# Kernel tuning notes

Measured on AMD Instinct MI355X. Metric: run time of the kernel, lower is better.

## Reference

```python
import jax, jax.numpy as jnp
import numpy as np

N, E, R = 50000, 500000, 3
IN, HID, OUT = 128, 128, 128
NEG_SLOPE = 0.2


def setup_inputs() -> dict:
    key = jax.random.key(0)
    ks = jax.random.split(key, 16)
    g = lambda i, shape: jax.random.normal(ks[i], shape, jnp.float32) * 0.1
    return {
        "x": jax.random.normal(ks[0], (N, IN), jnp.float32),
        "edge_index": jax.random.randint(ks[1], (2, E), 0, N, jnp.int32),
        "edge_type": jax.random.randint(ks[2], (E,), 0, R, jnp.int32),
        "edge_attr": jax.random.normal(ks[3], (E, 1), jnp.float32),
        # conv1 params (RGATConv: per-relation weight, q/k/e attention vectors, edge lin, bias)
        "w1": g(4, (R, IN, HID)), "q1": g(5, (HID, 1)), "k1": g(6, (HID, 1)),
        "le1": g(7, (1, HID)), "e1": g(8, (HID, 1)), "b1": jnp.zeros((HID,), jnp.float32),
        # conv2 params
        "w2": g(9, (R, HID, OUT)), "q2": g(10, (OUT, 1)), "k2": g(11, (OUT, 1)),
        "le2": g(12, (1, OUT)), "e2": g(13, (OUT, 1)), "b2": jnp.zeros((OUT,), jnp.float32),
    }


def _rgat_conv(x, src, dst, edge_type, edge_attr, w, q, k, le, e, b):
    """PyG RGATConv: heads=1, dim=1, additive-self-attention, across-relation softmax."""
    n = x.shape[0]
    # Per-relation linear at node level (equiv. to per-edge bmm with w[edge_type])
    xw = jnp.einsum('ni,rio->rno', x, w)            # [R, N, C]
    x_j = xw[edge_type, src]                          # [E, C] transformed source feats
    x_i = xw[edge_type, dst]                          # [E, C] transformed target feats
    # additive attention logits: q(x_i) + k(x_j) + e(lin_edge(edge_attr))
    alpha = x_i @ q + x_j @ k + (edge_attr @ le) @ e  # [E, 1]
    alpha = jax.nn.leaky_relu(alpha, negative_slope=NEG_SLOPE)
    # across-relation softmax over incoming edges of each target node
    amax = jax.ops.segment_max(alpha, dst, num_segments=n)
    amax = jnp.where(jnp.isfinite(amax), amax, 0.0)   # empty segments -> 0
    ex = jnp.exp(alpha - amax[dst])
    denom = jax.ops.segment_sum(ex, dst, num_segments=n)
    alpha = ex / (denom[dst] + 1e-16)
    # weighted scatter-add aggregation, then bias (concat=True, heads=1)
    out = jax.ops.segment_sum(alpha * x_j, dst, num_segments=n)  # [N, C]
    return out + b


def reference(x, edge_index, edge_type, edge_attr,
              w1, q1, k1, le1, e1, b1,
              w2, q2, k2, le2, e2, b2):
    src, dst = edge_index[0], edge_index[1]
    h = jax.nn.relu(_rgat_conv(x, src, dst, edge_type, edge_attr, w1, q1, k1, le1, e1, b1))
    return _rgat_conv(h, src, dst, edge_type, edge_attr, w2, q2, k2, le2, e2, b2)
```

## Files before the change

kernel.cpp:

```cpp
#include <hip/hip_runtime.h>
#include <hip/hip_bf16.h>
#include <math.h>

typedef __bf16 bf16x8 __attribute__((ext_vector_type(8)));
typedef float f32x4 __attribute__((ext_vector_type(4)));

#define CDIM 128

__global__ void sentinel_kernel(float* outf) {
  if (threadIdx.x == 0) outf[0] = 12345.0f;
}

__global__ __launch_bounds__(256) void prep_hist_kernel(
    const float* __restrict__ w1, const float* __restrict__ w2,
    __hip_bfloat16* __restrict__ wt,
    const float* __restrict__ le1, const float* __restrict__ e1,
    const float* __restrict__ le2, const float* __restrict__ e2,
    float* __restrict__ outc, const int* __restrict__ dstv,
    int* __restrict__ deg, int perW, int E) {
  const int b = blockIdx.x;
  const int tid = threadIdx.x;
  if (b < 48) {
    int t = b * 256 + tid;
    if (t >= perW * 2) return;
    const float* w = (t < perW) ? w1 : w2;
    int tt = (t < perW) ? t : t - perW;
    int r = tt >> 11;
    int rem = tt & 2047;
    int kb = rem >> 7;
    int o = rem & 127;
    const float* wr = w + ((size_t)r << 14);
    union { __hip_bfloat16 h[8]; int4 v; } u;
#pragma unroll
    for (int j = 0; j < 8; ++j)
      u.h[j] = __float2bfloat16(wr[(size_t)(kb * 8 + j) * CDIM + o]);
    *reinterpret_cast<int4*>(wt + (size_t)t * 8) = u.v;
  } else if (b == 48) {
    if (tid < 64) {
      float v1 = le1[tid] * e1[tid] + le1[tid + 64] * e1[tid + 64];
      float v2 = le2[tid] * e2[tid] + le2[tid + 64] * e2[tid + 64];
#pragma unroll
      for (int off = 32; off > 0; off >>= 1) {
        v1 += __shfl_xor(v1, off, 64);
        v2 += __shfl_xor(v2, off, 64);
      }
      if (tid == 0) { outc[0] = v1; outc[1] = v2; }
    }
  } else {
    int e0 = (b - 49) * 1024 + tid * 4;
    if (e0 + 3 < E) {
      int4 d4 = *reinterpret_cast<const int4*>(&dstv[e0]);
      atomicAdd(&deg[d4.x], 1);
      atomicAdd(&deg[d4.y], 1);
      atomicAdd(&deg[d4.z], 1);
      atomicAdd(&deg[d4.w], 1);
    } else {
      for (int t = 0; t < 4; ++t) {
        int e = e0 + t;
        if (e < E) atomicAdd(&deg[dstv[e]], 1);
      }
    }
  }
}


__global__ __launch_bounds__(256) void scan1_kernel(const int* __restrict__ deg,
                                                    int* __restrict__ rowptr,
                                                    int* __restrict__ partials, int n) {
  __shared__ int sh[256];
  int t = threadIdx.x;
  int base = blockIdx.x * 1024;
  int idx = base + t * 4;
  int v[4]; int s = 0;
#pragma unroll
  for (int j = 0; j < 4; ++j) { v[j] = (idx + j < n) ? deg[idx + j] : 0; s += v[j]; }
  sh[t] = s;
  __syncthreads();
  for (int off = 1; off < 256; off <<= 1) {
    int x = (t >= off) ? sh[t - off] : 0;
    __syncthreads();
    sh[t] += x;
    __syncthreads();
  }
  int excl = sh[t] - s;
  if (t == 255) partials[blockIdx.x] = sh[255];
  int run = excl;
#pragma unroll
  for (int j = 0; j < 4; ++j) {
    if (idx + j < n) rowptr[idx + j] = run;
    run += v[j];
  }
}

__global__ __launch_bounds__(256) void scan3_kernel(int* __restrict__ rowptr,
                                                    int* __restrict__ cursor,
                                                    const int* __restrict__ partials,
                                                    int nb, int n, int E) {
  __shared__ int spfx[64];
  int t = threadIdx.x;
  if (t < 64) {
    int pv = (t < nb) ? partials[t] : 0;
    int v = pv;
#pragma unroll
    for (int off = 1; off < 64; off <<= 1) {
      int u = __shfl_up(v, off, 64);
      if (t >= off) v += u;
    }
    spfx[t] = v - pv;
  }
  __syncthreads();
  int i = blockIdx.x * 256 + t;
  if (i < n) {
    int v = rowptr[i] + spfx[i >> 10];
    rowptr[i] = v;
    cursor[i] = v;
  } else if (i == n) {
    rowptr[n] = E;
  }
}

__device__ __forceinline__ void gemm_body64(
    int tb, const float* __restrict__ xin, const __hip_bfloat16* __restrict__ wt,
    const float* __restrict__ qv, const float* __restrict__ kv,
    __hip_bfloat16* __restrict__ xwout, float* __restrict__ sq,
    float* __restrict__ sk, int n, __hip_bfloat16* wlds, float* qls, float* kls) {
  const int tid = threadIdx.x;
  const int wave = tid >> 6, lane = tid & 63;
  const int quad = lane >> 4, c16 = lane & 15;
  const int m = tb * 64 + wave * 16 + c16;
  const bool ok = m < n;

  if (tid < 128) qls[tid] = qv[tid];
  else kls[tid - 128] = kv[tid - 128];

  bf16x8 zf;
#pragma unroll
  for (int j = 0; j < 8; ++j) zf[j] = (__bf16)0.0f;

  bf16x8 af[4];
#pragma unroll
  for (int ks = 0; ks < 4; ++ks) {
    if (ok) {
      const float* xp = xin + (size_t)m * CDIM + ks * 32 + quad * 8;
      f32x4 x0 = *reinterpret_cast<const f32x4*>(xp);
      f32x4 x1 = *reinterpret_cast<const f32x4*>(xp + 4);
      bf16x8 a;
#pragma unroll
      for (int j = 0; j < 4; ++j) { a[j] = (__bf16)x0[j]; a[4 + j] = (__bf16)x1[j]; }
      af[ks] = a;
    } else {
      af[ks] = zf;
    }
  }

  for (int r = 0; r < 3; ++r) {
    if (r) __syncthreads();
    {
      const int4* src = reinterpret_cast<const int4*>(wt + ((size_t)r << 14));
      int4* dst = reinterpret_cast<int4*>(wlds);
#pragma unroll
      for (int i = 0; i < 8; ++i) dst[tid + i * 256] = src[tid + i * 256];
    }
    __syncthreads();

    f32x4 acc[8];
#pragma unroll
    for (int ot = 0; ot < 8; ++ot) acc[ot] = (f32x4){0.f, 0.f, 0.f, 0.f};

#pragma unroll
    for (int ks = 0; ks < 4; ++ks) {
#pragma unroll
      for (int ot = 0; ot < 8; ++ot) {
        bf16x8 b = *reinterpret_cast<const bf16x8*>(
            &wlds[(((ks * 4 + quad) * 128) + ot * 16 + c16) * 8]);
        acc[ot] = __builtin_amdgcn_mfma_f32_16x16x32_bf16(b, af[ks], acc[ot], 0, 0, 0);
      }
    }

    __hip_bfloat16* rp = xwout + (((size_t)r * n + m) << 7) + quad * 4;
    float s_q = 0.f, s_k = 0.f;
#pragma unroll
    for (int ot = 0; ot < 8; ++ot) {
      f32x4 a = acc[ot];
      f32x4 q4 = *reinterpret_cast<const f32x4*>(&qls[ot * 16 + quad * 4]);
      f32x4 k4 = *reinterpret_cast<const f32x4*>(&kls[ot * 16 + quad * 4]);
      s_q += a[0] * q4[0] + a[1] * q4[1] + a[2] * q4[2] + a[3] * q4[3];
      s_k += a[0] * k4[0] + a[1] * k4[1] + a[2] * k4[2] + a[3] * k4[3];
      if (ok) {
        union { __hip_bfloat16 b4[4]; uint2 u; } pk;
#pragma unroll
        for (int t = 0; t < 4; ++t) pk.b4[t] = __float2bfloat16(a[t]);
        *reinterpret_cast<uint2*>(rp + ot * 16) = pk.u;
      }
    }
    s_q += __shfl_xor(s_q, 16, 64);
    s_q += __shfl_xor(s_q, 32, 64);
    s_k += __shfl_xor(s_k, 16, 64);
    s_k += __shfl_xor(s_k, 32, 64);
    if (quad == 0 && ok) {
      sq[(size_t)r * n + m] = s_q;
      sk[(size_t)r * n + m] = s_k;
    }
  }
}

__global__ __launch_bounds__(256) void gemm_scatter_kernel(
    const float* __restrict__ xin, const __hip_bfloat16* __restrict__ wt,
    const float* __restrict__ qv, const float* __restrict__ kv,
    __hip_bfloat16* __restrict__ xwout, float* __restrict__ sq, float* __restrict__ sk,
    const int* __restrict__ srcv, const int* __restrict__ dstv,
    const int* __restrict__ etype, const float* __restrict__ eattr,
    int* __restrict__ cursor, int2* __restrict__ kattr,
    int NT, int n, int E) {
  __shared__ __hip_bfloat16 wlds[16 * 128 * 8];
  __shared__ float qls[128], kls[128];
  const int b = blockIdx.x;
  if (b < NT) {
    gemm_body64(b, xin, wt, qv, kv, xwout, sq, sk, n, wlds, qls, kls);
  } else {
    int e0 = (b - NT) * 1024 + threadIdx.x * 4;
    if (e0 + 3 < E) {
      int4 s4 = *reinterpret_cast<const int4*>(&srcv[e0]);
      int4 d4 = *reinterpret_cast<const int4*>(&dstv[e0]);
      int4 t4 = *reinterpret_cast<const int4*>(&etype[e0]);
      float4 a4 = *reinterpret_cast<const float4*>(&eattr[e0]);
      int p0 = atomicAdd(&cursor[d4.x], 1);
      kattr[p0] = make_int2(t4.x * n + s4.x, __float_as_int(a4.x));
      int p1 = atomicAdd(&cursor[d4.y], 1);
      kattr[p1] = make_int2(t4.y * n + s4.y, __float_as_int(a4.y));
      int p2 = atomicAdd(&cursor[d4.z], 1);
      kattr[p2] = make_int2(t4.z * n + s4.z, __float_as_int(a4.z));
      int p3 = atomicAdd(&cursor[d4.w], 1);
      kattr[p3] = make_int2(t4.w * n + s4.w, __float_as_int(a4.w));
    } else {
      for (int t = 0; t < 4; ++t) {
        int e = e0 + t;
        if (e < E) {
          int p = atomicAdd(&cursor[dstv[e]], 1);
          kattr[p] = make_int2(etype[e] * n + srcv[e], __float_as_int(eattr[e]));
        }
      }
    }
  }
}

__global__ __launch_bounds__(256) void gemm_xw_kernel(
    const float* __restrict__ xin, const __hip_bfloat16* __restrict__ wt,
    const float* __restrict__ qv, const float* __restrict__ kv,
    __hip_bfloat16* __restrict__ xwout, float* __restrict__ sq, float* __restrict__ sk,
    int n) {
  __shared__ __hip_bfloat16 wlds[16 * 128 * 8];
  __shared__ float qls[128], kls[128];
  gemm_body64(blockIdx.x, xin, wt, qv, kv, xwout, sq, sk, n, wlds, qls, kls);
}

__global__ __launch_bounds__(256) void aggregate_kernel(
    const int* __restrict__ rowptr, const int2* __restrict__ kattr,
    const float* __restrict__ sq, const float* __restrict__ sk,
    const __hip_bfloat16* __restrict__ xw, const float* __restrict__ bias,
    const float* __restrict__ cscal, float* __restrict__ out, int n, int do_relu) {
  const int wave = threadIdx.x >> 6, lane = threadIdx.x & 63;
  const int g = lane >> 4;
  const int sub = lane & 15;
  const int node = blockIdx.x * 16 + wave * 4 + g;
  if (node >= n) return;
  const float c = cscal[0];
  const int n2 = n * 2;

  const int start = rowptr[node];
  const int deg = rowptr[node + 1] - start;
  const float s0 = sq[node], s1 = sq[n + node], s2 = sq[n2 + node];

  float acc[8];
#pragma unroll
  for (int t = 0; t < 8; ++t) acc[t] = 0.f;
  float den = 0.f;

  for (int j0 = 0; j0 < deg; j0 += 4) {
    int2 ka[4];
#pragma unroll
    for (int t = 0; t < 4; ++t) {
      int idx = j0 + t;
      ka[t] = kattr[start + (idx < deg ? idx : 0)];
    }
    float w[4];
    bf16x8 f[4];
#pragma unroll
    for (int t = 0; t < 4; ++t) {
      int kk = ka[t].x;
      float sv = (kk >= n2) ? s2 : ((kk >= n) ? s1 : s0);
      float l = sv + sk[kk] + c * __int_as_float(ka[t].y);
      l = l > 0.f ? l : 0.2f * l;
      w[t] = (j0 + t < deg) ? __expf(l) : 0.f;
      f[t] = *reinterpret_cast<const bf16x8*>(xw + ((size_t)kk << 7) + sub * 8);
    }
#pragma unroll
    for (int t = 0; t < 8; ++t)
      acc[t] += w[0] * (float)f[0][t] + w[1] * (float)f[1][t] +
                w[2] * (float)f[2][t] + w[3] * (float)f[3][t];
    den += (w[0] + w[1]) + (w[2] + w[3]);
  }

  float inv = 1.0f / (den + 1e-16f);
  f32x4 b0 = *reinterpret_cast<const f32x4*>(bias + sub * 8);
  f32x4 b1 = *reinterpret_cast<const f32x4*>(bias + sub * 8 + 4);
  f32x4 o0, o1;
#pragma unroll
  for (int t = 0; t < 4; ++t) {
    o0[t] = acc[t] * inv + b0[t];
    o1[t] = acc[4 + t] * inv + b1[t];
  }
  if (do_relu) {
#pragma unroll
    for (int t = 0; t < 4; ++t) {
      o0[t] = fmaxf(o0[t], 0.f);
      o1[t] = fmaxf(o1[t], 0.f);
    }
  }
  float* op = out + (size_t)node * CDIM + sub * 8;
  *reinterpret_cast<f32x4*>(op) = o0;
  *reinterpret_cast<f32x4*>(op + 4) = o1;
}


extern "C" void kernel_launch(void* const* d_in, const int* in_sizes, int n_in,
                              void* d_out, int out_size, void* d_ws, size_t ws_size,
                              hipStream_t stream) {
  const float* x     = (const float*)d_in[0];
  const int*   eidx  = (const int*)d_in[1];
  const int*   etype = (const int*)d_in[2];
  const float* eattr = (const float*)d_in[3];
  const float* w1  = (const float*)d_in[4];
  const float* q1  = (const float*)d_in[5];
  const float* k1  = (const float*)d_in[6];
  const float* le1 = (const float*)d_in[7];
  const float* e1  = (const float*)d_in[8];
  const float* b1  = (const float*)d_in[9];
  const float* w2  = (const float*)d_in[10];
  const float* q2  = (const float*)d_in[11];
  const float* k2  = (const float*)d_in[12];
  const float* le2 = (const float*)d_in[13];
  const float* e2  = (const float*)d_in[14];
  const float* b2  = (const float*)d_in[15];

  const int N = in_sizes[0] / CDIM;
  const int E = in_sizes[2];
  const int R = in_sizes[4] / (CDIM * CDIM);
  const int* srcv = eidx;
  const int* dstv = eidx + E;

  char* p = (char*)d_ws;
  auto alloc = [&](size_t bytes) -> void* {
    void* q = (void*)p;
    p += (bytes + 255) & ~(size_t)255;
    return q;
  };
  float* sq       = (float*)alloc((size_t)R * N * 4);
  float* sk       = (float*)alloc((size_t)R * N * 4);
  int*   deg      = (int*)alloc((size_t)N * 4);
  int*   rowptr   = (int*)alloc((size_t)(N + 1) * 4);
  int*   cursor   = (int*)alloc((size_t)N * 4);
  int*   partials = (int*)alloc(4096);
  int2*  kattr    = (int2*)alloc((size_t)E * 8);
  __hip_bfloat16* wt = (__hip_bfloat16*)alloc((size_t)2 * R * CDIM * CDIM * 2);
  float* cscal    = (float*)alloc(256);
  __hip_bfloat16* xw = (__hip_bfloat16*)alloc((size_t)R * N * CDIM * 2);

  size_t needed = (size_t)(p - (char*)d_ws);
  if (needed > ws_size) {
    sentinel_kernel<<<1, 64, 0, stream>>>((float*)d_out);
    return;
  }

  float* outp = (float*)d_out;
  float* hbuf = outp;

  const int eg4 = (E + 1023) / 1024;
  const int nb = (N + 1023) / 1024;
  const int NT = (N + 63) / 64;
  const int nodes16 = (N + 15) / 16;
  const int perW = R * 2048;

  hipMemsetAsync(deg, 0, (size_t)N * 4, stream);

  prep_hist_kernel<<<49 + eg4, 256, 0, stream>>>(w1, w2, wt, le1, e1, le2, e2,
                                                 cscal, dstv, deg, perW, E);

  scan1_kernel<<<nb, 256, 0, stream>>>(deg, rowptr, partials, N);
  scan3_kernel<<<(N + 1 + 255) / 256, 256, 0, stream>>>(rowptr, cursor, partials, nb, N, E);

  gemm_scatter_kernel<<<NT + eg4, 256, 0, stream>>>(x, wt, q1, k1, xw, sq, sk,
                                                    srcv, dstv, etype, eattr,
                                                    cursor, kattr, NT, N, E);

  aggregate_kernel<<<nodes16, 256, 0, stream>>>(rowptr, kattr, sq, sk, xw, b1,
                                                cscal + 0, hbuf, N, 1);

  gemm_xw_kernel<<<NT, 256, 0, stream>>>(hbuf, wt + (size_t)R * CDIM * CDIM,
                                         q2, k2, xw, sq, sk, N);

  aggregate_kernel<<<nodes16, 256, 0, stream>>>(rowptr, kattr, sq, sk, xw, b2,
                                                cscal + 1, outp, N, 0);
}
```

Measured before the change: 248.1 us.

## Store hidden layer in bf16, split scatter from gemm, prefetch edge records

The first-layer aggregate now writes the ReLU'd hidden features as bf16 into a workspace buffer, and the second GEMM reads bf16 directly. This halves the intermediate write and read traffic and drops a conversion. The fused gemm+scatter kernel is split into two separate launches, which adds a launch and removes the overlap between the two workloads. The aggregate loop software-prefetches the next group of four edge records before computing the current group.

```diff
diff --git a/kernel.cpp b/kernel.cpp
--- a/kernel.cpp
+++ b/kernel.cpp
@@ -119,8 +119,39 @@
   }
 }
 
+__global__ __launch_bounds__(256) void scatter_kernel(
+    const int* __restrict__ srcv, const int* __restrict__ dstv,
+    const int* __restrict__ etype, const float* __restrict__ eattr,
+    int* __restrict__ cursor, int2* __restrict__ kattr, int E, int n) {
+  int e0 = blockIdx.x * 1024 + threadIdx.x * 4;
+  if (e0 + 3 < E) {
+    int4 s4 = *reinterpret_cast<const int4*>(&srcv[e0]);
+    int4 d4 = *reinterpret_cast<const int4*>(&dstv[e0]);
+    int4 t4 = *reinterpret_cast<const int4*>(&etype[e0]);
+    float4 a4 = *reinterpret_cast<const float4*>(&eattr[e0]);
+    int p0 = atomicAdd(&cursor[d4.x], 1);
+    kattr[p0] = make_int2(t4.x * n + s4.x, __float_as_int(a4.x));
+    int p1 = atomicAdd(&cursor[d4.y], 1);
+    kattr[p1] = make_int2(t4.y * n + s4.y, __float_as_int(a4.y));
+    int p2 = atomicAdd(&cursor[d4.z], 1);
+    kattr[p2] = make_int2(t4.z * n + s4.z, __float_as_int(a4.z));
+    int p3 = atomicAdd(&cursor[d4.w], 1);
+    kattr[p3] = make_int2(t4.w * n + s4.w, __float_as_int(a4.w));
+  } else {
+    for (int t = 0; t < 4; ++t) {
+      int e = e0 + t;
+      if (e < E) {
+        int p = atomicAdd(&cursor[dstv[e]], 1);
+        kattr[p] = make_int2(etype[e] * n + srcv[e], __float_as_int(eattr[e]));
+      }
+    }
+  }
+}
+
+template <int BF16IN>
 __device__ __forceinline__ void gemm_body64(
-    int tb, const float* __restrict__ xin, const __hip_bfloat16* __restrict__ wt,
+    int tb, const float* __restrict__ xf, const __hip_bfloat16* __restrict__ xb,
+    const __hip_bfloat16* __restrict__ wt,
     const float* __restrict__ qv, const float* __restrict__ kv,
     __hip_bfloat16* __restrict__ xwout, float* __restrict__ sq,
     float* __restrict__ sk, int n, __hip_bfloat16* wlds, float* qls, float* kls) {
@@ -141,13 +172,18 @@
 #pragma unroll
   for (int ks = 0; ks < 4; ++ks) {
     if (ok) {
-      const float* xp = xin + (size_t)m * CDIM + ks * 32 + quad * 8;
-      f32x4 x0 = *reinterpret_cast<const f32x4*>(xp);
-      f32x4 x1 = *reinterpret_cast<const f32x4*>(xp + 4);
-      bf16x8 a;
-#pragma unroll
-      for (int j = 0; j < 4; ++j) { a[j] = (__bf16)x0[j]; a[4 + j] = (__bf16)x1[j]; }
-      af[ks] = a;
+      if (BF16IN) {
+        af[ks] = *reinterpret_cast<const bf16x8*>(
+            xb + (size_t)m * CDIM + ks * 32 + quad * 8);
+      } else {
+        const float* xp = xf + (size_t)m * CDIM + ks * 32 + quad * 8;
+        f32x4 x0 = *reinterpret_cast<const f32x4*>(xp);
+        f32x4 x1 = *reinterpret_cast<const f32x4*>(xp + 4);
+        bf16x8 a;
+#pragma unroll
+        for (int j = 0; j < 4; ++j) { a[j] = (__bf16)x0[j]; a[4 + j] = (__bf16)x1[j]; }
+        af[ks] = a;
+      }
     } else {
       af[ks] = zf;
     }
@@ -204,61 +240,35 @@
   }
 }
 
-__global__ __launch_bounds__(256) void gemm_scatter_kernel(
-    const float* __restrict__ xin, const __hip_bfloat16* __restrict__ wt,
-    const float* __restrict__ qv, const float* __restrict__ kv,
-    __hip_bfloat16* __restrict__ xwout, float* __restrict__ sq, float* __restrict__ sk,
-    const int* __restrict__ srcv, const int* __restrict__ dstv,
-    const int* __restrict__ etype, const float* __restrict__ eattr,
-    int* __restrict__ cursor, int2* __restrict__ kattr,
-    int NT, int n, int E) {
-  __shared__ __hip_bfloat16 wlds[16 * 128 * 8];
-  __shared__ float qls[128], kls[128];
-  const int b = blockIdx.x;
-  if (b < NT) {
-    gemm_body64(b, xin, wt, qv, kv, xwout, sq, sk, n, wlds, qls, kls);
-  } else {
-    int e0 = (b - NT) * 1024 + threadIdx.x * 4;
-    if (e0 + 3 < E) {
-      int4 s4 = *reinterpret_cast<const int4*>(&srcv[e0]);
-      int4 d4 = *reinterpret_cast<const int4*>(&dstv[e0]);
-      int4 t4 = *reinterpret_cast<const int4*>(&etype[e0]);
-      float4 a4 = *reinterpret_cast<const float4*>(&eattr[e0]);
-      int p0 = atomicAdd(&cursor[d4.x], 1);
-      kattr[p0] = make_int2(t4.x * n + s4.x, __float_as_int(a4.x));
-      int p1 = atomicAdd(&cursor[d4.y], 1);
-      kattr[p1] = make_int2(t4.y * n + s4.y, __float_as_int(a4.y));
-      int p2 = atomicAdd(&cursor[d4.z], 1);
-      kattr[p2] = make_int2(t4.z * n + s4.z, __float_as_int(a4.z));
-      int p3 = atomicAdd(&cursor[d4.w], 1);
-      kattr[p3] = make_int2(t4.w * n + s4.w, __float_as_int(a4.w));
-    } else {
-      for (int t = 0; t < 4; ++t) {
-        int e = e0 + t;
-        if (e < E) {
-          int p = atomicAdd(&cursor[dstv[e]], 1);
-          kattr[p] = make_int2(etype[e] * n + srcv[e], __float_as_int(eattr[e]));
-        }
-      }
-    }
-  }
-}
-
-__global__ __launch_bounds__(256) void gemm_xw_kernel(
+__global__ __launch_bounds__(256) void gemm_xw_f32_kernel(
     const float* __restrict__ xin, const __hip_bfloat16* __restrict__ wt,
     const float* __restrict__ qv, const float* __restrict__ kv,
     __hip_bfloat16* __restrict__ xwout, float* __restrict__ sq, float* __restrict__ sk,
     int n) {
   __shared__ __hip_bfloat16 wlds[16 * 128 * 8];
   __shared__ float qls[128], kls[128];
-  gemm_body64(blockIdx.x, xin, wt, qv, kv, xwout, sq, sk, n, wlds, qls, kls);
-}
-
+  gemm_body64<0>(blockIdx.x, xin, nullptr, wt, qv, kv, xwout, sq, sk, n,
+                 wlds, qls, kls);
+}
+
+__global__ __launch_bounds__(256) void gemm_xw_bf16_kernel(
+    const __hip_bfloat16* __restrict__ xin, const __hip_bfloat16* __restrict__ wt,
+    const float* __restrict__ qv, const float* __restrict__ kv,
+    __hip_bfloat16* __restrict__ xwout, float* __restrict__ sq, float* __restrict__ sk,
+    int n) {
+  __shared__ __hip_bfloat16 wlds[16 * 128 * 8];
+  __shared__ float qls[128], kls[128];
+  gemm_body64<1>(blockIdx.x, nullptr, xin, wt, qv, kv, xwout, sq, sk, n,
+                 wlds, qls, kls);
+}
+
+template <int OUTBF16>
 __global__ __launch_bounds__(256) void aggregate_kernel(
     const int* __restrict__ rowptr, const int2* __restrict__ kattr,
     const float* __restrict__ sq, const float* __restrict__ sk,
     const __hip_bfloat16* __restrict__ xw, const float* __restrict__ bias,
-    const float* __restrict__ cscal, float* __restrict__ out, int n, int do_relu) {
+    const float* __restrict__ cscal, float* __restrict__ outf,
+    __hip_bfloat16* __restrict__ outb, int n) {
   const int wave = threadIdx.x >> 6, lane = threadIdx.x & 63;
   const int g = lane >> 4;
   const int sub = lane & 15;
@@ -276,29 +286,39 @@
   for (int t = 0; t < 8; ++t) acc[t] = 0.f;
   float den = 0.f;
 
-  for (int j0 = 0; j0 < deg; j0 += 4) {
-    int2 ka[4];
-#pragma unroll
-    for (int t = 0; t < 4; ++t) {
-      int idx = j0 + t;
-      ka[t] = kattr[start + (idx < deg ? idx : 0)];
-    }
-    float w[4];
-    bf16x8 f[4];
-#pragma unroll
-    for (int t = 0; t < 4; ++t) {
-      int kk = ka[t].x;
-      float sv = (kk >= n2) ? s2 : ((kk >= n) ? s1 : s0);
-      float l = sv + sk[kk] + c * __int_as_float(ka[t].y);
-      l = l > 0.f ? l : 0.2f * l;
-      w[t] = (j0 + t < deg) ? __expf(l) : 0.f;
-      f[t] = *reinterpret_cast<const bf16x8*>(xw + ((size_t)kk << 7) + sub * 8);
-    }
-#pragma unroll
-    for (int t = 0; t < 8; ++t)
-      acc[t] += w[0] * (float)f[0][t] + w[1] * (float)f[1][t] +
-                w[2] * (float)f[2][t] + w[3] * (float)f[3][t];
-    den += (w[0] + w[1]) + (w[2] + w[3]);
+  if (deg > 0) {
+    int2 kaA0, kaA1, kaA2, kaA3;
+    kaA0 = kattr[start + (0 < deg ? 0 : 0)];
+    kaA1 = kattr[start + (1 < deg ? 1 : 0)];
+    kaA2 = kattr[start + (2 < deg ? 2 : 0)];
+    kaA3 = kattr[start + (3 < deg ? 3 : 0)];
+    for (int j0 = 0; j0 < deg; j0 += 4) {
+      int nj = j0 + 4;
+      int2 kaB0 = kattr[start + (nj + 0 < deg ? nj + 0 : 0)];
+      int2 kaB1 = kattr[start + (nj + 1 < deg ? nj + 1 : 0)];
+      int2 kaB2 = kattr[start + (nj + 2 < deg ? nj + 2 : 0)];
+      int2 kaB3 = kattr[start + (nj + 3 < deg ? nj + 3 : 0)];
+
+      int2 ka[4] = {kaA0, kaA1, kaA2, kaA3};
+      float w[4];
+      bf16x8 f[4];
+#pragma unroll
+      for (int t = 0; t < 4; ++t) {
+        int kk = ka[t].x;
+        float sv = (kk >= n2) ? s2 : ((kk >= n) ? s1 : s0);
+        float l = sv + sk[kk] + c * __int_as_float(ka[t].y);
+        l = l > 0.f ? l : 0.2f * l;
+        w[t] = (j0 + t < deg) ? __expf(l) : 0.f;
+        f[t] = *reinterpret_cast<const bf16x8*>(xw + ((size_t)kk << 7) + sub * 8);
+      }
+#pragma unroll
+      for (int t = 0; t < 8; ++t)
+        acc[t] += w[0] * (float)f[0][t] + w[1] * (float)f[1][t] +
+                  w[2] * (float)f[2][t] + w[3] * (float)f[3][t];
+      den += (w[0] + w[1]) + (w[2] + w[3]);
+
+      kaA0 = kaB0; kaA1 = kaB1; kaA2 = kaB2; kaA3 = kaB3;
+    }
   }
 
   float inv = 1.0f / (den + 1e-16f);
@@ -310,16 +330,19 @@
     o0[t] = acc[t] * inv + b0[t];
     o1[t] = acc[4 + t] * inv + b1[t];
   }
-  if (do_relu) {
+  if (OUTBF16) {
+    union { __hip_bfloat16 h[8]; int4 v; } pk;
 #pragma unroll
     for (int t = 0; t < 4; ++t) {
-      o0[t] = fmaxf(o0[t], 0.f);
-      o1[t] = fmaxf(o1[t], 0.f);
-    }
-  }
-  float* op = out + (size_t)node * CDIM + sub * 8;
-  *reinterpret_cast<f32x4*>(op) = o0;
-  *reinterpret_cast<f32x4*>(op + 4) = o1;
+      pk.h[t] = __float2bfloat16(fmaxf(o0[t], 0.f));
+      pk.h[4 + t] = __float2bfloat16(fmaxf(o1[t], 0.f));
+    }
+    *reinterpret_cast<int4*>(outb + (size_t)node * CDIM + sub * 8) = pk.v;
+  } else {
+    float* op = outf + (size_t)node * CDIM + sub * 8;
+    *reinterpret_cast<f32x4*>(op) = o0;
+    *reinterpret_cast<f32x4*>(op + 4) = o1;
+  }
 }
 
 
@@ -365,6 +388,7 @@
   __hip_bfloat16* wt = (__hip_bfloat16*)alloc((size_t)2 * R * CDIM * CDIM * 2);
   float* cscal    = (float*)alloc(256);
   __hip_bfloat16* xw = (__hip_bfloat16*)alloc((size_t)R * N * CDIM * 2);
+  __hip_bfloat16* hb = (__hip_bfloat16*)alloc((size_t)N * CDIM * 2);
 
   size_t needed = (size_t)(p - (char*)d_ws);
   if (needed > ws_size) {
@@ -373,7 +397,6 @@
   }
 
   float* outp = (float*)d_out;
-  float* hbuf = outp;
 
   const int eg4 = (E + 1023) / 1024;
   const int nb = (N + 1023) / 1024;
@@ -389,16 +412,16 @@
   scan1_kernel<<<nb, 256, 0, stream>>>(deg, rowptr, partials, N);
   scan3_kernel<<<(N + 1 + 255) / 256, 256, 0, stream>>>(rowptr, cursor, partials, nb, N, E);
 
-  gemm_scatter_kernel<<<NT + eg4, 256, 0, stream>>>(x, wt, q1, k1, xw, sq, sk,
-                                                    srcv, dstv, etype, eattr,
-                                                    cursor, kattr, NT, N, E);
-
-  aggregate_kernel<<<nodes16, 256, 0, stream>>>(rowptr, kattr, sq, sk, xw, b1,
-                                                cscal + 0, hbuf, N, 1);
-
-  gemm_xw_kernel<<<NT, 256, 0, stream>>>(hbuf, wt + (size_t)R * CDIM * CDIM,
-                                         q2, k2, xw, sq, sk, N);
-
-  aggregate_kernel<<<nodes16, 256, 0, stream>>>(rowptr, kattr, sq, sk, xw, b2,
-                                                cscal + 1, outp, N, 0);
-}
+  scatter_kernel<<<eg4, 256, 0, stream>>>(srcv, dstv, etype, eattr, cursor, kattr, E, N);
+
+  gemm_xw_f32_kernel<<<NT, 256, 0, stream>>>(x, wt, q1, k1, xw, sq, sk, N);
+
+  aggregate_kernel<1><<<nodes16, 256, 0, stream>>>(rowptr, kattr, sq, sk, xw, b1,
+                                                   cscal + 0, nullptr, hb, N);
+
+  gemm_xw_bf16_kernel<<<NT, 256, 0, stream>>>(hb, wt + (size_t)R * CDIM * CDIM,
+                                              q2, k2, xw, sq, sk, N);
+
+  aggregate_kernel<0><<<nodes16, 256, 0, stream>>>(rowptr, kattr, sq, sk, xw, b2,
+                                                   cscal + 1, outp, nullptr, N);
+}
```

Result: slower. 257.4 us (+3.7%).
